# Performance work log

Measured on AMD Instinct MI355X. Metric: run time of the kernel, lower is better.

## Reference

```python
import jax, jax.numpy as jnp
import numpy as np

# ---- static config (from xib add_argument defaults / chosen production sizes) ----
B, L = 16, 50            # batch, text length
LU, KU, DIM = 60, 100, 60
V, MAXVL = 2000, 10      # vocab size, max vocab word length (J)
MIN_WL, MAX_WL = 4, 10   # min/max extracted word length
NE = MAX_WL - MIN_WL + 1 # number of len_e candidates
INS_DEL_COST = 3.5       # min_ins_del_cost
UNEXTRACTED_PROB = 0.01
CONTEXT_WEIGHT = 0.1     # weight for context (conv) log-probs
NEG = -9999.9


def setup_inputs() -> dict:
    key = jax.random.key(0)
    ks = jax.random.split(key, 8)
    unit_id_seqs = jax.random.randint(ks[0], (B, L), 0, LU)
    lengths = 10 + jax.random.randint(ks[1], (B,), 0, L - 9)  # in [10, L]
    unit_repr = jax.random.normal(ks[2], (KU, DIM), jnp.float32)
    aligner_weight = 0.1 * jax.random.normal(ks[3], (LU, KU), jnp.float32)
    conv_w = jax.random.normal(ks[4], (DIM, DIM, 3), jnp.float32) / np.sqrt(3.0 * DIM)
    conv_b = jnp.zeros((DIM,), jnp.float32)
    vocab_ids = jax.random.randint(ks[5], (V, MAXVL), 0, KU)
    vocab_lengths = MIN_WL + jax.random.randint(ks[6], (V,), 0, MAXVL - MIN_WL + 1)
    return dict(unit_id_seqs=unit_id_seqs, lengths=lengths, unit_repr=unit_repr,
                aligner_weight=aligner_weight, conv_w=conv_w, conv_b=conv_b,
                vocab_ids=vocab_ids, vocab_lengths=vocab_lengths)


def reference(unit_id_seqs, lengths, unit_repr, aligner_weight, conv_w, conv_b,
              vocab_ids, vocab_lengths):
    # ---- G2P layer: embedding-as-matmul + Conv1d over length ----
    ku_char_repr = aligner_weight @ unit_repr                 # (LU, DIM)
    emb = ku_char_repr[unit_id_seqs]                          # (B, L, DIM)
    x = jnp.swapaxes(emb, 1, 2)                               # (B, DIM, L)
    y = jax.lax.conv_general_dilated(x, conv_w, (1,), 'SAME',
                                     dimension_numbers=('NCH', 'OIH', 'NCH'))
    word_repr = jnp.swapaxes(y + conv_b[None, :, None], 1, 2)  # (B, L, DIM)
    char_log_probs = jax.nn.log_softmax(ku_char_repr @ unit_repr.T, axis=-1)  # (LU, KU)
    alignment = jnp.exp(char_log_probs)
    ctx_log_probs = jax.nn.log_softmax(word_repr @ unit_repr.T, axis=-1)      # (B, L, KU)
    # per-position substitution log prob against each known unit
    pos_lp = char_log_probs[unit_id_seqs] + CONTEXT_WEIGHT * ctx_log_probs    # (B, L, KU)
    sub = pos_lp[:, :, vocab_ids]                                             # (B, L, V, J)
    sub = jnp.pad(sub, ((0, 0), (0, MAX_WL), (0, 0), (0, 0)), constant_values=NEG)
    J = MAXVL
    # ---- edit-distance style DP over (span char i, vocab char j), vectorized
    # over (batch, start position, vocab). prev[b,s,j,v] = f[i-1][j].
    j_ar = jnp.arange(J + 1, dtype=sub.dtype)
    prev = jnp.broadcast_to((-INS_DEL_COST * j_ar)[None, None, :, None], (B, L, J + 1, V))
    vl_idx = jnp.broadcast_to(vocab_lengths[None, None, None, :].astype(jnp.int32), (B, L, 1, V))
    lls = []
    for i in range(1, MAX_WL + 1):          # fixed small loop (<=10)
        sub_i = sub[:, i - 1:i - 1 + L]     # (B, L, V, J): char at position s+i-1
        row = [jnp.full((B, L, V), -INS_DEL_COST * i, dtype=sub.dtype)]
        for j in range(1, J + 1):           # fixed small loop (<=10)
            diag = prev[:, :, j - 1, :] + sub_i[:, :, :, j - 1]
            up = prev[:, :, j, :] - INS_DEL_COST
            left = row[j - 1] - INS_DEL_COST
            row.append(jnp.maximum(diag, jnp.maximum(up, left)))
        prev = jnp.stack(row, axis=2)       # (B, L, J+1, V)
        if i >= MIN_WL:                     # matched ll for word length i
            lls.append(jnp.take_along_axis(prev, vl_idx, axis=2)[:, :, 0, :])
    ll = jnp.stack(lls, axis=2)             # (B, L, NE, V) = matches.ll
    # ---- viability mask + unextracted penalty, pick best candidate ----
    starts = jnp.arange(L)
    word_lens = MIN_WL + jnp.arange(NE)
    viable = (starts[None, :, None] + word_lens[None, None, :]) <= lengths[:, None, None]  # (B,L,NE)
    unextracted = (lengths[:, None, None] - word_lens[None, None, :]).astype(ll.dtype)     # (B,1,NE)
    score = (ll + jnp.where(viable, 0.0, NEG)[..., None]
             + (unextracted * np.log(UNEXTRACTED_PROB))[..., None, :, None][:, 0])
    flat = score.reshape(B, L * NE * V)
    best_idx = jnp.argmax(flat, axis=1)
    best_matched_ll = jnp.max(flat, axis=1)
    start = best_idx // (NE * V)
    e_idx = (best_idx // V) % NE
    best_matched_vocab = best_idx % V
    end = start + MIN_WL + e_idx - 1
    return start, end, best_matched_ll, best_matched_vocab, alignment
```

## Files before the change

### kernel.cpp

```cpp
#include <hip/hip_runtime.h>
#include <math.h>
#include <stdint.h>

#define B_ 16
#define L_ 50
#define LU_ 60
#define KU_ 100
#define DIM_ 60
#define V_ 2000
#define MAXVL_ 10
#define MIN_WL_ 4
#define MAX_WL_ 10
#define NE_ 7
#define IDC_ 3.5f
#define LOG_UNEXT_ (-4.6051701859880913680359829093687f)
#define CTXW_ 0.1f
#define NQ_ 13

#define WS_PLP  0
#define WS_BEST_BYTES (80000u * 4u)
#define BEST_STRIDE 8
#define WS_VPACK_BYTES (WS_BEST_BYTES + 1024u)

#define URP_ 61
#define CWP_ 61
#define SP2_ 208

__global__ __launch_bounds__(256) void ctx_kernel(
    const int* __restrict__ uid,
    const float* __restrict__ unit_repr,
    const float* __restrict__ aligner_w,
    const float* __restrict__ conv_w,
    const float* __restrict__ conv_b,
    const int* __restrict__ vocab_ids,
    const int* __restrict__ vocab_lengths,
    float* __restrict__ ws_plp,
    float* __restrict__ out_align,
    unsigned long long* __restrict__ g_best,
    int* __restrict__ vpack)
{
  int blk = blockIdx.x;
  int t = threadIdx.x;

  if (blk == B_ * NQ_) {
    __shared__ unsigned scnt[NE_];
    if (t < NE_) scnt[t] = 0u;
    __syncthreads();
    for (int v = t; v < V_; v += 256)
      atomicAdd(&scnt[vocab_lengths[v] - MIN_WL_], 1u);
    __syncthreads();
    if (t == 0) {
      unsigned s = 0;
      for (int e = 0; e < NE_; ++e) { unsigned c = scnt[e]; scnt[e] = s; s += c; }
    }
    __syncthreads();
    for (int v = t; v < V_; v += 256) {
      int vl = vocab_lengths[v];
      unsigned dst = atomicAdd(&scnt[vl - MIN_WL_], 1u);
      unsigned q0 = 0u, q1 = 0u, q2 = 0u;
#pragma unroll
      for (int j = 0; j < 4; ++j) q0 |= ((unsigned)vocab_ids[v * MAXVL_ + j]) << (j * 8);
#pragma unroll
      for (int j = 0; j < 4; ++j) q1 |= ((unsigned)vocab_ids[v * MAXVL_ + 4 + j]) << (j * 8);
#pragma unroll
      for (int j = 0; j < 2; ++j) q2 |= ((unsigned)vocab_ids[v * MAXVL_ + 8 + j]) << (j * 8);
      int4 w;
      w.x = (int)q0; w.y = (int)q1; w.z = (int)q2;
      w.w = (int)((unsigned)vl | ((unsigned)v << 8));
      ((int4*)vpack)[dst] = w;
    }
    return;
  }

  int b = blk / NQ_, q = blk % NQ_;
  int l0 = 4 * q;
  int npos = (l0 + 4 <= L_) ? 4 : (L_ - l0);
  int alr = (blk < LU_) ? blk : -1;

  __shared__ float s_ur[KU_ * URP_];
  __shared__ float s_cw[3 * DIM_ * CWP_];
  __shared__ float s_aw[7 * KU_];
  __shared__ float s_kx[7 * DIM_];
  __shared__ float swr[4 * DIM_];
  __shared__ float sclp[4 * KU_];
  __shared__ float sctx[4 * KU_];
  __shared__ float salg[KU_];
  __shared__ float sls[9];

  if (blk == 0 && t < B_) g_best[t * BEST_STRIDE] = 0ull;

  const float4* ur4 = (const float4*)unit_repr;
  for (int k = t; k < (KU_ * DIM_) / 4; k += 256) {
    float4 v = ur4[k];
    int i0 = 4 * k;
    s_ur[((i0 + 0) / DIM_) * URP_ + ((i0 + 0) % DIM_)] = v.x;
    s_ur[((i0 + 1) / DIM_) * URP_ + ((i0 + 1) % DIM_)] = v.y;
    s_ur[((i0 + 2) / DIM_) * URP_ + ((i0 + 2) % DIM_)] = v.z;
    s_ur[((i0 + 3) / DIM_) * URP_ + ((i0 + 3) % DIM_)] = v.w;
  }
  const float4* cw4 = (const float4*)conv_w;
  for (int k = t; k < (DIM_ * DIM_ * 3) / 4; k += 256) {
    float4 v = cw4[k];
    int i0 = 4 * k;
    float vv[4] = {v.x, v.y, v.z, v.w};
#pragma unroll
    for (int e = 0; e < 4; ++e) {
      int idx = i0 + e;
      int o = idx / (3 * DIM_), id = idx % (3 * DIM_);
      s_cw[id * CWP_ + o] = vv[e];
    }
  }
  for (int i = t; i < 7 * KU_; i += 256) {
    int m = i / KU_, k = i - m * KU_;
    float w = 0.f;
    if (m < 6) {
      int ld = l0 - 1 + m;
      if (ld >= 0 && ld < L_) {
        int u = uid[b * L_ + ld];
        w = aligner_w[u * KU_ + k];
      }
    } else if (alr >= 0) {
      w = aligner_w[alr * KU_ + k];
    }
    s_aw[i] = w;
  }
  __syncthreads();

  for (int idx = t; idx < 7 * DIM_; idx += 256) {
    int m = idx / DIM_, c = idx - m * DIM_;
    const float4* aw4 = (const float4*)&s_aw[m * KU_];
    float acc = 0.f;
    for (int k4 = 0; k4 < KU_ / 4; ++k4) {
      float4 a = aw4[k4];
      int k = 4 * k4;
      acc += a.x * s_ur[(k + 0) * URP_ + c];
      acc += a.y * s_ur[(k + 1) * URP_ + c];
      acc += a.z * s_ur[(k + 2) * URP_ + c];
      acc += a.w * s_ur[(k + 3) * URP_ + c];
    }
    s_kx[idx] = acc;
  }
  __syncthreads();

  for (int idx = t; idx < 240 + 4 * KU_; idx += 256) {
    if (idx < 240) {
      int p = idx / DIM_, o = idx - p * DIM_;
      const float4* x04 = (const float4*)&s_kx[(p + 0) * DIM_];
      const float4* x14 = (const float4*)&s_kx[(p + 1) * DIM_];
      const float4* x24 = (const float4*)&s_kx[(p + 2) * DIM_];
      float acc = conv_b[o];
      for (int i4 = 0; i4 < DIM_ / 4; ++i4) {
        float4 x0 = x04[i4], x1 = x14[i4], x2 = x24[i4];
        int i = 4 * i4;
        acc += x0.x * s_cw[((i + 0) * 3 + 0) * CWP_ + o];
        acc += x1.x * s_cw[((i + 0) * 3 + 1) * CWP_ + o];
        acc += x2.x * s_cw[((i + 0) * 3 + 2) * CWP_ + o];
        acc += x0.y * s_cw[((i + 1) * 3 + 0) * CWP_ + o];
        acc += x1.y * s_cw[((i + 1) * 3 + 1) * CWP_ + o];
        acc += x2.y * s_cw[((i + 1) * 3 + 2) * CWP_ + o];
        acc += x0.z * s_cw[((i + 2) * 3 + 0) * CWP_ + o];
        acc += x1.z * s_cw[((i + 2) * 3 + 1) * CWP_ + o];
        acc += x2.z * s_cw[((i + 2) * 3 + 2) * CWP_ + o];
        acc += x0.w * s_cw[((i + 3) * 3 + 0) * CWP_ + o];
        acc += x1.w * s_cw[((i + 3) * 3 + 1) * CWP_ + o];
        acc += x2.w * s_cw[((i + 3) * 3 + 2) * CWP_ + o];
      }
      swr[p * DIM_ + o] = acc;
    } else {
      int r = idx - 240;
      int p = r / KU_, j = r - p * KU_;
      const float4* kx4 = (const float4*)&s_kx[(p + 1) * DIM_];
      float acc = 0.f;
      for (int d4 = 0; d4 < DIM_ / 4; ++d4) {
        float4 x = kx4[d4];
        int d = 4 * d4;
        acc += x.x * s_ur[j * URP_ + d + 0];
        acc += x.y * s_ur[j * URP_ + d + 1];
        acc += x.z * s_ur[j * URP_ + d + 2];
        acc += x.w * s_ur[j * URP_ + d + 3];
      }
      sclp[r] = acc;
    }
  }
  __syncthreads();

  for (int idx = t; idx < 4 * KU_ + KU_; idx += 256) {
    if (idx < 4 * KU_) {
      int p = idx / KU_, j = idx - p * KU_;
      const float4* w4 = (const float4*)&swr[p * DIM_];
      float acc = 0.f;
      for (int d4 = 0; d4 < DIM_ / 4; ++d4) {
        float4 x = w4[d4];
        int d = 4 * d4;
        acc += x.x * s_ur[j * URP_ + d + 0];
        acc += x.y * s_ur[j * URP_ + d + 1];
        acc += x.z * s_ur[j * URP_ + d + 2];
        acc += x.w * s_ur[j * URP_ + d + 3];
      }
      sctx[idx] = acc;
    } else {
      int j = idx - 4 * KU_;
      const float4* kx4 = (const float4*)&s_kx[6 * DIM_];
      float acc = 0.f;
      for (int d4 = 0; d4 < DIM_ / 4; ++d4) {
        float4 x = kx4[d4];
        int d = 4 * d4;
        acc += x.x * s_ur[j * URP_ + d + 0];
        acc += x.y * s_ur[j * URP_ + d + 1];
        acc += x.z * s_ur[j * URP_ + d + 2];
        acc += x.w * s_ur[j * URP_ + d + 3];
      }
      salg[j] = acc;
    }
  }
  __syncthreads();

  {
    int g = t >> 5, lane = t & 31;
#pragma unroll
    for (int round = 0; round < 2; ++round) {
      int r = round * 8 + g;
      if (r < 9) {
        const float* arr = (r == 8) ? salg
                          : ((r & 1) ? &sctx[(r >> 1) * KU_] : &sclp[(r >> 1) * KU_]);
        float v1 = arr[lane];
        float v2 = arr[32 + lane];
        float v3 = arr[64 + lane];
        float v4 = (lane < KU_ - 96) ? arr[96 + lane] : -1e30f;
        float mx = fmaxf(fmaxf(v1, v2), fmaxf(v3, v4));
#pragma unroll
        for (int off = 16; off > 0; off >>= 1)
          mx = fmaxf(mx, __shfl_xor(mx, off));
        float s = expf(v1 - mx) + expf(v2 - mx) + expf(v3 - mx) +
                  ((lane < KU_ - 96) ? expf(v4 - mx) : 0.f);
#pragma unroll
        for (int off = 16; off > 0; off >>= 1)
          s += __shfl_xor(s, off);
        if (lane == 0) sls[r] = mx + logf(s);
      }
    }
  }
  __syncthreads();

  for (int idx = t; idx < 4 * KU_; idx += 256) {
    int p = idx / KU_, j = idx - p * KU_;
    if (p < npos) {
      float pos = (sclp[idx] - sls[2 * p]) + CTXW_ * (sctx[idx] - sls[2 * p + 1]);
      ws_plp[(b * L_ + l0 + p) * KU_ + j] = pos + 2.0f * IDC_;
    }
  }
  if (alr >= 0 && t < KU_)
    out_align[alr * KU_ + t] = expf(salg[t] - sls[8]);
}

template<int VL>
__device__ __forceinline__ unsigned long long dp_one(
    const float* __restrict__ spair, const int* koff8,
    int imax, int len_b, int l, int v)
{
  float D[VL + 1];
#pragma unroll
  for (int j = 0; j <= VL; ++j) D[j] = 0.f;
  float bestSc = -1e30f;
  int bestI = 0;
  const char* sb = (const char*)spair;

#pragma unroll
  for (int r2 = 0; r2 < 5; ++r2) {
    const int i1 = 2 * r2 + 1, i2 = 2 * r2 + 2;
    if (i1 <= imax) {
      float2 pv[VL];
#pragma unroll
      for (int j = 0; j < VL; ++j)
        pv[j] = *(const float2*)(sb + r2 * (SP2_ * 4) + koff8[j]);
      float left = 0.f;
#pragma unroll
      for (int j = 1; j <= VL; ++j) {
        float nv = fmaxf(D[j - 1] + pv[j - 1].x, fmaxf(D[j], left));
        D[j - 1] = left;
        left = nv;
      }
      D[VL] = left;
      if (i1 >= MIN_WL_) {
        float sc = left + ((float)(len_b - i1) * LOG_UNEXT_ - IDC_ * (float)(i1 + VL));
        if (sc > bestSc) { bestSc = sc; bestI = i1; }
      }
      if (i2 <= imax) {
        left = 0.f;
#pragma unroll
        for (int j = 1; j <= VL; ++j) {
          float nv = fmaxf(D[j - 1] + pv[j - 1].y, fmaxf(D[j], left));
          D[j - 1] = left;
          left = nv;
        }
        D[VL] = left;
        if (i2 >= MIN_WL_) {
          float sc = left + ((float)(len_b - i2) * LOG_UNEXT_ - IDC_ * (float)(i2 + VL));
          if (sc > bestSc) { bestSc = sc; bestI = i2; }
        }
      }
    }
  }
  if (bestI == 0) return 0ull;
  unsigned idx = (unsigned)(l * (NE_ * V_) + (bestI - MIN_WL_) * V_ + v);
  unsigned u = __float_as_uint(bestSc);
  u = (u & 0x80000000u) ? ~u : (u | 0x80000000u);
  return ((unsigned long long)u << 32) | (unsigned long long)(~idx);
}

__global__ __launch_bounds__(256) void dp_kernel(
    const int* __restrict__ lengths,
    const float* __restrict__ ws_plp,
    const int* __restrict__ vpack,
    unsigned long long* __restrict__ g_best)
{
  int bl = blockIdx.x;
  int b = bl / L_, l = bl % L_;
  int len_b = lengths[b];
  int imax = len_b - l;
  if (imax > MAX_WL_) imax = MAX_WL_;
  if (imax < MIN_WL_) return;

  __shared__ float spair[5 * SP2_];
  __shared__ unsigned long long swave[4];
  int t = threadIdx.x;
  if (t < 250) {
    const float4* src = (const float4*)(ws_plp + (size_t)bl * KU_);
    int r = t / 25, m = t - r * 25;
    float4 v = src[r * 25 + m];
    int r2 = r >> 1, h = r & 1;
    float* dst = &spair[r2 * SP2_ + 8 * m + h];
    dst[0] = v.x; dst[2] = v.y; dst[4] = v.z; dst[6] = v.w;
  }
  __syncthreads();

  int p = blockIdx.y * 256 + t;
  const int4* vp4 = (const int4*)vpack;
  int4 w0 = (p < V_) ? vp4[p] : make_int4(0, 0, 0, 0);
  int vlen = (int)((unsigned)w0.w & 0xFFu);
  int v0 = (int)(((unsigned)w0.w) >> 8);

  int koff8[MAXVL_];
  {
    unsigned q[3] = {(unsigned)w0.x, (unsigned)w0.y, (unsigned)w0.z};
#pragma unroll
    for (int j = 0; j < MAXVL_; ++j)
      koff8[j] = (int)((q[j >> 2] >> ((j & 3) * 8)) & 0xFFu) * 8;
  }

  unsigned long long bestKey = 0ull;
  if (vlen == 4)       bestKey = dp_one<4>(spair, koff8, imax, len_b, l, v0);
  else if (vlen == 5)  bestKey = dp_one<5>(spair, koff8, imax, len_b, l, v0);
  else if (vlen == 6)  bestKey = dp_one<6>(spair, koff8, imax, len_b, l, v0);
  else if (vlen == 7)  bestKey = dp_one<7>(spair, koff8, imax, len_b, l, v0);
  else if (vlen == 8)  bestKey = dp_one<8>(spair, koff8, imax, len_b, l, v0);
  else if (vlen == 9)  bestKey = dp_one<9>(spair, koff8, imax, len_b, l, v0);
  else if (vlen == 10) bestKey = dp_one<10>(spair, koff8, imax, len_b, l, v0);

#pragma unroll
  for (int off = 32; off > 0; off >>= 1) {
    unsigned long long o = __shfl_down(bestKey, off);
    if (o > bestKey) bestKey = o;
  }
  int wid = t >> 6;
  if ((t & 63) == 0) swave[wid] = bestKey;
  __syncthreads();
  if (t == 0) {
    unsigned long long k0 = swave[0];
    for (int w = 1; w < 4; ++w)
      if (swave[w] > k0) k0 = swave[w];
    atomicMax(g_best + (size_t)b * BEST_STRIDE, k0);
  }
}

__global__ void decode_kernel(const unsigned long long* __restrict__ g_best,
                              float* __restrict__ out)
{
  int t = threadIdx.x;
  if (t < B_) {
    unsigned long long key = g_best[t * BEST_STRIDE];
    unsigned int u = (unsigned int)(key >> 32);
    unsigned int idx = ~((unsigned int)(key & 0xFFFFFFFFull));
    unsigned int bits = (u & 0x80000000u) ? (u & 0x7FFFFFFFu) : ~u;
    float val = __uint_as_float(bits);
    int start = (int)(idx / (NE_ * V_));
    int rem = (int)(idx % (NE_ * V_));
    int e = rem / V_;
    int vv = rem % V_;
    out[t] = (float)start;
    out[B_ + t] = (float)(start + MIN_WL_ + e - 1);
    out[2 * B_ + t] = val;
    out[3 * B_ + t] = (float)vv;
  }
}

extern "C" void kernel_launch(void* const* d_in, const int* in_sizes, int n_in,
                              void* d_out, int out_size, void* d_ws, size_t ws_size,
                              hipStream_t stream)
{
  const int* uid            = (const int*)d_in[0];
  const int* lengths        = (const int*)d_in[1];
  const float* unit_repr    = (const float*)d_in[2];
  const float* aligner_w    = (const float*)d_in[3];
  const float* conv_w       = (const float*)d_in[4];
  const float* conv_b       = (const float*)d_in[5];
  const int* vocab_ids      = (const int*)d_in[6];
  const int* vocab_lengths  = (const int*)d_in[7];
  float* out = (float*)d_out;
  float* ws_f = (float*)d_ws;
  unsigned long long* g_best =
      (unsigned long long*)((char*)d_ws + WS_BEST_BYTES);
  int* vpack = (int*)((char*)d_ws + WS_VPACK_BYTES);

  ctx_kernel<<<B_ * NQ_ + 1, 256, 0, stream>>>(uid, unit_repr, aligner_w,
                                               conv_w, conv_b, vocab_ids,
                                               vocab_lengths, ws_f + WS_PLP,
                                               out + 4 * B_, g_best, vpack);
  dim3 g3(B_ * L_, 8);
  dp_kernel<<<g3, 256, 0, stream>>>(lengths, ws_f + WS_PLP, vpack, g_best);
  decode_kernel<<<1, 64, 0, stream>>>(g_best, out);
}
```

Measured before the change: 102.0 us.

## Remap DP so lanes cover start positions and waves iterate vocab words

The DP kernel now launches one block per batch row and vocab chunk. Each of the 64 lanes handles one start position, and each wave loops over ten vocab words that are uniform across the wave (loaded via readfirstlane). This removes the divergence from per-thread vocab lengths, so the length-sorting prepass is dropped and vpack is written in original order. The DP is transposed to iterate over vocab characters against all 10 text positions, and a precomputed per-lane score vector handles length viability and the unextracted penalty. In exchange each block stages 54 rows of position log-probs into shared memory, DP work runs past each row's valid length, and 14 of the 64 lanes are idle.

```diff
diff --git a/kernel.cpp b/kernel.cpp
--- a/kernel.cpp
+++ b/kernel.cpp
@@ -24,7 +24,9 @@
 
 #define URP_ 61
 #define CWP_ 61
-#define SP2_ 208
+
+#define S2_ 202
+#define NKEY_ 54
 
 __global__ __launch_bounds__(256) void ctx_kernel(
     const int* __restrict__ uid,
@@ -43,20 +45,8 @@
   int t = threadIdx.x;
 
   if (blk == B_ * NQ_) {
-    __shared__ unsigned scnt[NE_];
-    if (t < NE_) scnt[t] = 0u;
-    __syncthreads();
-    for (int v = t; v < V_; v += 256)
-      atomicAdd(&scnt[vocab_lengths[v] - MIN_WL_], 1u);
-    __syncthreads();
-    if (t == 0) {
-      unsigned s = 0;
-      for (int e = 0; e < NE_; ++e) { unsigned c = scnt[e]; scnt[e] = s; s += c; }
-    }
-    __syncthreads();
     for (int v = t; v < V_; v += 256) {
       int vl = vocab_lengths[v];
-      unsigned dst = atomicAdd(&scnt[vl - MIN_WL_], 1u);
       unsigned q0 = 0u, q1 = 0u, q2 = 0u;
 #pragma unroll
       for (int j = 0; j < 4; ++j) q0 |= ((unsigned)vocab_ids[v * MAXVL_ + j]) << (j * 8);
@@ -67,7 +57,7 @@
       int4 w;
       w.x = (int)q0; w.y = (int)q1; w.z = (int)q2;
       w.w = (int)((unsigned)vl | ((unsigned)v << 8));
-      ((int4*)vpack)[dst] = w;
+      ((int4*)vpack)[v] = w;
     }
     return;
   }
@@ -255,57 +245,49 @@
 
 template<int VL>
 __device__ __forceinline__ unsigned long long dp_one(
-    const float* __restrict__ spair, const int* koff8,
-    int imax, int len_b, int l, int v)
+    const float* __restrict__ fb,
+    unsigned q0, unsigned q1, unsigned q2,
+    const float* cvec, int lbase, int vid)
 {
-  float D[VL + 1];
-#pragma unroll
-  for (int j = 0; j <= VL; ++j) D[j] = 0.f;
+  float D[MAXVL_ + 1];
+#pragma unroll
+  for (int i = 0; i <= MAXVL_; ++i) D[i] = 0.f;
+
+#pragma unroll
+  for (int j = 0; j < VL; ++j) {
+    unsigned qq = (j < 4) ? q0 : ((j < 8) ? q1 : q2);
+    int k2 = (int)((qq >> ((j & 3) * 8)) & 0xFFu) * 2;
+    float2 p0 = *(const float2*)(fb + k2);
+    float2 p1 = *(const float2*)(fb + k2 + S2_);
+    float2 p2 = *(const float2*)(fb + k2 + 2 * S2_);
+    float2 p3 = *(const float2*)(fb + k2 + 3 * S2_);
+    float2 p4 = *(const float2*)(fb + k2 + 4 * S2_);
+    float s[MAXVL_] = {p0.x, p1.x, p2.x, p3.x, p4.x,
+                       p0.y, p1.y, p2.y, p3.y, p4.y};
+    float left = 0.f;
+#pragma unroll
+    for (int i = 1; i <= MAXVL_; ++i) {
+      float nv = fmaxf(D[i - 1] + s[i - 1], fmaxf(D[i], left));
+      D[i - 1] = left;
+      left = nv;
+    }
+    D[MAXVL_] = left;
+  }
+
   float bestSc = -1e30f;
-  int bestI = 0;
-  const char* sb = (const char*)spair;
-
-#pragma unroll
-  for (int r2 = 0; r2 < 5; ++r2) {
-    const int i1 = 2 * r2 + 1, i2 = 2 * r2 + 2;
-    if (i1 <= imax) {
-      float2 pv[VL];
-#pragma unroll
-      for (int j = 0; j < VL; ++j)
-        pv[j] = *(const float2*)(sb + r2 * (SP2_ * 4) + koff8[j]);
-      float left = 0.f;
-#pragma unroll
-      for (int j = 1; j <= VL; ++j) {
-        float nv = fmaxf(D[j - 1] + pv[j - 1].x, fmaxf(D[j], left));
-        D[j - 1] = left;
-        left = nv;
-      }
-      D[VL] = left;
-      if (i1 >= MIN_WL_) {
-        float sc = left + ((float)(len_b - i1) * LOG_UNEXT_ - IDC_ * (float)(i1 + VL));
-        if (sc > bestSc) { bestSc = sc; bestI = i1; }
-      }
-      if (i2 <= imax) {
-        left = 0.f;
-#pragma unroll
-        for (int j = 1; j <= VL; ++j) {
-          float nv = fmaxf(D[j - 1] + pv[j - 1].y, fmaxf(D[j], left));
-          D[j - 1] = left;
-          left = nv;
-        }
-        D[VL] = left;
-        if (i2 >= MIN_WL_) {
-          float sc = left + ((float)(len_b - i2) * LOG_UNEXT_ - IDC_ * (float)(i2 + VL));
-          if (sc > bestSc) { bestSc = sc; bestI = i2; }
-        }
-      }
-    }
-  }
-  if (bestI == 0) return 0ull;
-  unsigned idx = (unsigned)(l * (NE_ * V_) + (bestI - MIN_WL_) * V_ + v);
+  int bestEV = 0;
+#pragma unroll
+  for (int e = 0; e < NE_; ++e) {
+    float sc = D[MIN_WL_ + e] + cvec[e];
+    if (sc > bestSc) { bestSc = sc; bestEV = e * V_; }
+  }
+  bestSc -= IDC_ * (float)VL;
+  unsigned idx = (unsigned)(lbase + bestEV + vid);
   unsigned u = __float_as_uint(bestSc);
   u = (u & 0x80000000u) ? ~u : (u | 0x80000000u);
-  return ((unsigned long long)u << 32) | (unsigned long long)(~idx);
+  unsigned long long key =
+      ((unsigned long long)u << 32) | (unsigned long long)(~idx);
+  return (bestSc > -1e29f) ? key : 0ull;
 }
 
 __global__ __launch_bounds__(256) void dp_kernel(
@@ -314,61 +296,77 @@
     const int* __restrict__ vpack,
     unsigned long long* __restrict__ g_best)
 {
-  int bl = blockIdx.x;
-  int b = bl / L_, l = bl % L_;
+  __shared__ float sp[NKEY_ * S2_];
+  __shared__ unsigned long long swave[4];
+  int b = blockIdx.x;
+  int chunk = blockIdx.y;
+  int t = threadIdx.x;
   int len_b = lengths[b];
-  int imax = len_b - l;
-  if (imax > MAX_WL_) imax = MAX_WL_;
-  if (imax < MIN_WL_) return;
-
-  __shared__ float spair[5 * SP2_];
-  __shared__ unsigned long long swave[4];
-  int t = threadIdx.x;
-  if (t < 250) {
-    const float4* src = (const float4*)(ws_plp + (size_t)bl * KU_);
-    int r = t / 25, m = t - r * 25;
-    float4 v = src[r * 25 + m];
-    int r2 = r >> 1, h = r & 1;
-    float* dst = &spair[r2 * SP2_ + 8 * m + h];
-    dst[0] = v.x; dst[2] = v.y; dst[4] = v.z; dst[6] = v.w;
-  }
-  __syncthreads();
-
-  int p = blockIdx.y * 256 + t;
+
+  const float4* src4 = (const float4*)ws_plp;
+  for (int idx = t; idx < NKEY_ * 25; idx += 256) {
+    int key = idx / 25, m = idx - key * 25;
+    int ra = b * L_ + key;     if (ra > B_ * L_ - 1) ra = B_ * L_ - 1;
+    int rb = b * L_ + key + 5; if (rb > B_ * L_ - 1) rb = B_ * L_ - 1;
+    float4 qa = src4[ra * 25 + m];
+    float4 qb = src4[rb * 25 + m];
+    float2* dst = (float2*)&sp[key * S2_ + 8 * m];
+    dst[0] = make_float2(qa.x, qb.x);
+    dst[1] = make_float2(qa.y, qb.y);
+    dst[2] = make_float2(qa.z, qb.z);
+    dst[3] = make_float2(qa.w, qb.w);
+  }
+
+  int lane = t & 63, w = t >> 6;
+  float cvec[NE_];
+#pragma unroll
+  for (int e = 0; e < NE_; ++e) {
+    int i = MIN_WL_ + e;
+    bool ok = (lane < L_) && (i <= len_b - lane);
+    cvec[e] = ok ? ((float)(len_b - i) * LOG_UNEXT_ - IDC_ * (float)i) : -1e30f;
+  }
+  int lbase = lane * (NE_ * V_);
+  int lcl = (lane < L_) ? lane : (L_ - 1);
+  const float* fb = sp + lcl * S2_;
+  __syncthreads();
+
+  unsigned long long bestKey = 0ull;
   const int4* vp4 = (const int4*)vpack;
-  int4 w0 = (p < V_) ? vp4[p] : make_int4(0, 0, 0, 0);
-  int vlen = (int)((unsigned)w0.w & 0xFFu);
-  int v0 = (int)(((unsigned)w0.w) >> 8);
-
-  int koff8[MAXVL_];
-  {
-    unsigned q[3] = {(unsigned)w0.x, (unsigned)w0.y, (unsigned)w0.z};
-#pragma unroll
-    for (int j = 0; j < MAXVL_; ++j)
-      koff8[j] = (int)((q[j >> 2] >> ((j & 3) * 8)) & 0xFFu) * 8;
-  }
-
-  unsigned long long bestKey = 0ull;
-  if (vlen == 4)       bestKey = dp_one<4>(spair, koff8, imax, len_b, l, v0);
-  else if (vlen == 5)  bestKey = dp_one<5>(spair, koff8, imax, len_b, l, v0);
-  else if (vlen == 6)  bestKey = dp_one<6>(spair, koff8, imax, len_b, l, v0);
-  else if (vlen == 7)  bestKey = dp_one<7>(spair, koff8, imax, len_b, l, v0);
-  else if (vlen == 8)  bestKey = dp_one<8>(spair, koff8, imax, len_b, l, v0);
-  else if (vlen == 9)  bestKey = dp_one<9>(spair, koff8, imax, len_b, l, v0);
-  else if (vlen == 10) bestKey = dp_one<10>(spair, koff8, imax, len_b, l, v0);
+#pragma unroll 1
+  for (int n = 0; n < 10; ++n) {
+    int v = chunk * 40 + w * 10 + n;
+    int4 wq = vp4[v];
+    unsigned q0 = (unsigned)__builtin_amdgcn_readfirstlane(wq.x);
+    unsigned q1 = (unsigned)__builtin_amdgcn_readfirstlane(wq.y);
+    unsigned q2 = (unsigned)__builtin_amdgcn_readfirstlane(wq.z);
+    unsigned q3 = (unsigned)__builtin_amdgcn_readfirstlane(wq.w);
+    int vlen = (int)(q3 & 0xFFu);
+    int vid = (int)(q3 >> 8);
+    unsigned long long kk = 0ull;
+    switch (vlen) {
+      case 4:  kk = dp_one<4>(fb, q0, q1, q2, cvec, lbase, vid); break;
+      case 5:  kk = dp_one<5>(fb, q0, q1, q2, cvec, lbase, vid); break;
+      case 6:  kk = dp_one<6>(fb, q0, q1, q2, cvec, lbase, vid); break;
+      case 7:  kk = dp_one<7>(fb, q0, q1, q2, cvec, lbase, vid); break;
+      case 8:  kk = dp_one<8>(fb, q0, q1, q2, cvec, lbase, vid); break;
+      case 9:  kk = dp_one<9>(fb, q0, q1, q2, cvec, lbase, vid); break;
+      case 10: kk = dp_one<10>(fb, q0, q1, q2, cvec, lbase, vid); break;
+      default: break;
+    }
+    if (kk > bestKey) bestKey = kk;
+  }
 
 #pragma unroll
   for (int off = 32; off > 0; off >>= 1) {
     unsigned long long o = __shfl_down(bestKey, off);
     if (o > bestKey) bestKey = o;
   }
-  int wid = t >> 6;
-  if ((t & 63) == 0) swave[wid] = bestKey;
+  if ((t & 63) == 0) swave[w] = bestKey;
   __syncthreads();
   if (t == 0) {
     unsigned long long k0 = swave[0];
-    for (int w = 1; w < 4; ++w)
-      if (swave[w] > k0) k0 = swave[w];
+    for (int x = 1; x < 4; ++x)
+      if (swave[x] > k0) k0 = swave[x];
     atomicMax(g_best + (size_t)b * BEST_STRIDE, k0);
   }
 }
@@ -416,7 +414,7 @@
                                                conv_w, conv_b, vocab_ids,
                                                vocab_lengths, ws_f + WS_PLP,
                                                out + 4 * B_, g_best, vpack);
-  dim3 g3(B_ * L_, 8);
+  dim3 g3(B_, 50);
   dp_kernel<<<g3, 256, 0, stream>>>(lengths, ws_f + WS_PLP, vpack, g_best);
   decode_kernel<<<1, 64, 0, stream>>>(g_best, out);
 }
```

After: 106.4 us. 4.4% more time.

## Process four start positions per thread with transposed DP over vocab chars

Applied to the files above, without the earlier changes.

Restructures the edit-distance DP so each thread handles one vocab word against four consecutive start positions at once, iterating over vocab characters in the outer loop and reusing each shared-memory pair load across four DP chains. Blocks now cover a (batch, 4-start) tile with 512 threads, each looping over four vocab words with a prefetch of the next word's packed ids. This cuts the grid from 6400 blocks to 208 and amortises the log-prob loads and the vocab metadata reads. In exchange, register pressure rises because four DP arrays are live, and the fixed MAXVL-length chains do extra work for short words. Occupancy is also lower with so few blocks.

```diff
diff --git a/kernel.cpp b/kernel.cpp
--- a/kernel.cpp
+++ b/kernel.cpp
@@ -24,7 +24,9 @@
 
 #define URP_ 61
 #define CWP_ 61
-#define SP2_ 208
+
+#define S2P_ 208
+#define NROW_ 14
 
 __global__ __launch_bounds__(256) void ctx_kernel(
     const int* __restrict__ uid,
@@ -253,109 +255,126 @@
     out_align[alr * KU_ + t] = expf(salg[t] - sls[8]);
 }
 
+#define CHAIN_(Dm, MOFF)                                                 \
+  {                                                                      \
+    float left = 0.f;                                                    \
+    _Pragma("unroll")                                                    \
+    for (int i = 1; i <= MAXVL_; ++i) {                                  \
+      float nv = fmaxf(Dm[i - 1] + s[(i - 1) + (MOFF)],                  \
+                       fmaxf(Dm[i], left));                              \
+      Dm[i - 1] = left;                                                  \
+      left = nv;                                                         \
+    }                                                                    \
+    Dm[MAXVL_] = left;                                                   \
+  }
+
 template<int VL>
-__device__ __forceinline__ unsigned long long dp_one(
-    const float* __restrict__ spair, const int* koff8,
-    int imax, int len_b, int l, int v)
+__device__ __forceinline__ unsigned long long dp4_one(
+    const float* __restrict__ sp,
+    unsigned q0, unsigned q1, unsigned q2,
+    int imax0,
+    float lenLU,
+    int lbase0, int vid)
 {
-  float D[VL + 1];
-#pragma unroll
-  for (int j = 0; j <= VL; ++j) D[j] = 0.f;
-  float bestSc = -1e30f;
-  int bestI = 0;
-  const char* sb = (const char*)spair;
-
-#pragma unroll
-  for (int r2 = 0; r2 < 5; ++r2) {
-    const int i1 = 2 * r2 + 1, i2 = 2 * r2 + 2;
-    if (i1 <= imax) {
-      float2 pv[VL];
-#pragma unroll
-      for (int j = 0; j < VL; ++j)
-        pv[j] = *(const float2*)(sb + r2 * (SP2_ * 4) + koff8[j]);
-      float left = 0.f;
-#pragma unroll
-      for (int j = 1; j <= VL; ++j) {
-        float nv = fmaxf(D[j - 1] + pv[j - 1].x, fmaxf(D[j], left));
-        D[j - 1] = left;
-        left = nv;
-      }
-      D[VL] = left;
-      if (i1 >= MIN_WL_) {
-        float sc = left + ((float)(len_b - i1) * LOG_UNEXT_ - IDC_ * (float)(i1 + VL));
-        if (sc > bestSc) { bestSc = sc; bestI = i1; }
-      }
-      if (i2 <= imax) {
-        left = 0.f;
-#pragma unroll
-        for (int j = 1; j <= VL; ++j) {
-          float nv = fmaxf(D[j - 1] + pv[j - 1].y, fmaxf(D[j], left));
-          D[j - 1] = left;
-          left = nv;
-        }
-        D[VL] = left;
-        if (i2 >= MIN_WL_) {
-          float sc = left + ((float)(len_b - i2) * LOG_UNEXT_ - IDC_ * (float)(i2 + VL));
-          if (sc > bestSc) { bestSc = sc; bestI = i2; }
-        }
-      }
-    }
-  }
-  if (bestI == 0) return 0ull;
-  unsigned idx = (unsigned)(l * (NE_ * V_) + (bestI - MIN_WL_) * V_ + v);
-  unsigned u = __float_as_uint(bestSc);
-  u = (u & 0x80000000u) ? ~u : (u | 0x80000000u);
-  return ((unsigned long long)u << 32) | (unsigned long long)(~idx);
+  float D0[MAXVL_ + 1], D1[MAXVL_ + 1], D2[MAXVL_ + 1], D3[MAXVL_ + 1];
+#pragma unroll
+  for (int i = 0; i <= MAXVL_; ++i) { D0[i] = 0.f; D1[i] = 0.f; D2[i] = 0.f; D3[i] = 0.f; }
+
+#pragma unroll
+  for (int j = 0; j < VL; ++j) {
+    unsigned qq = (j < 4) ? q0 : ((j < 8) ? q1 : q2);
+    int k2 = (int)((qq >> ((j & 3) * 8)) & 0xFFu) * 2;
+    const float* fb = sp + k2;
+    float2 P0 = *(const float2*)(fb);
+    float2 P1 = *(const float2*)(fb + S2P_);
+    float2 P2 = *(const float2*)(fb + 2 * S2P_);
+    float2 P3 = *(const float2*)(fb + 3 * S2P_);
+    float2 P4 = *(const float2*)(fb + 4 * S2P_);
+    float2 P5 = *(const float2*)(fb + 5 * S2P_);
+    float2 P6 = *(const float2*)(fb + 6 * S2P_);
+    float s[NROW_] = {P0.x, P0.y, P1.x, P1.y, P2.x, P2.y, P3.x, P3.y,
+                      P4.x, P4.y, P5.x, P5.y, P6.x, P6.y};
+    CHAIN_(D0, 0)
+    CHAIN_(D1, 1)
+    CHAIN_(D2, 2)
+    CHAIN_(D3, 3)
+  }
+
+  unsigned long long bestKey = 0ull;
+#pragma unroll
+  for (int m = 0; m < 4; ++m) {
+    const float* Dm = (m == 0) ? D0 : (m == 1) ? D1 : (m == 2) ? D2 : D3;
+    int imax = imax0 - m;
+#pragma unroll
+    for (int e = 0; e < NE_; ++e) {
+      const int i = MIN_WL_ + e;
+      if (i <= imax) {
+        float cc = lenLU + (float)i * (-LOG_UNEXT_ - IDC_) - IDC_ * (float)VL;
+        float sc = Dm[i] + cc;
+        unsigned idx = (unsigned)(lbase0 + m * (NE_ * V_) + e * V_ + vid);
+        unsigned u = __float_as_uint(sc);
+        u = (u & 0x80000000u) ? ~u : (u | 0x80000000u);
+        unsigned long long key =
+            ((unsigned long long)u << 32) | (unsigned long long)(~idx);
+        if (key > bestKey) bestKey = key;
+      }
+    }
+  }
+  return bestKey;
 }
 
-__global__ __launch_bounds__(256) void dp_kernel(
+__global__ __launch_bounds__(512) void dp_kernel(
     const int* __restrict__ lengths,
     const float* __restrict__ ws_plp,
     const int* __restrict__ vpack,
     unsigned long long* __restrict__ g_best)
 {
-  int bl = blockIdx.x;
-  int b = bl / L_, l = bl % L_;
+  int blk = blockIdx.x;
+  int b = blk / NQ_, q = blk % NQ_;
+  int l0 = 4 * q;
   int len_b = lengths[b];
-  int imax = len_b - l;
-  if (imax > MAX_WL_) imax = MAX_WL_;
-  if (imax < MIN_WL_) return;
-
-  __shared__ float spair[5 * SP2_];
-  __shared__ unsigned long long swave[4];
+  int imax0 = len_b - l0;
+  if (imax0 < MIN_WL_) return;
+
+  __shared__ float sp[7 * S2P_];
+  __shared__ unsigned long long swave[8];
   int t = threadIdx.x;
-  if (t < 250) {
-    const float4* src = (const float4*)(ws_plp + (size_t)bl * KU_);
-    int r = t / 25, m = t - r * 25;
-    float4 v = src[r * 25 + m];
-    int r2 = r >> 1, h = r & 1;
-    float* dst = &spair[r2 * SP2_ + 8 * m + h];
+
+  if (t < NROW_ * 25) {
+    const float4* src4 = (const float4*)ws_plp;
+    int r = t / 25, m4 = t - r * 25;
+    int g = b * L_ + l0 + r;
+    if (g > B_ * L_ - 1) g = B_ * L_ - 1;
+    float4 v = src4[g * 25 + m4];
+    float* dst = &sp[(r >> 1) * S2P_ + 8 * m4 + (r & 1)];
     dst[0] = v.x; dst[2] = v.y; dst[4] = v.z; dst[6] = v.w;
   }
   __syncthreads();
 
-  int p = blockIdx.y * 256 + t;
+  float lenLU = (float)len_b * LOG_UNEXT_;
+  int lbase0 = l0 * (NE_ * V_);
   const int4* vp4 = (const int4*)vpack;
-  int4 w0 = (p < V_) ? vp4[p] : make_int4(0, 0, 0, 0);
-  int vlen = (int)((unsigned)w0.w & 0xFFu);
-  int v0 = (int)(((unsigned)w0.w) >> 8);
-
-  int koff8[MAXVL_];
-  {
-    unsigned q[3] = {(unsigned)w0.x, (unsigned)w0.y, (unsigned)w0.z};
-#pragma unroll
-    for (int j = 0; j < MAXVL_; ++j)
-      koff8[j] = (int)((q[j >> 2] >> ((j & 3) * 8)) & 0xFFu) * 8;
-  }
 
   unsigned long long bestKey = 0ull;
-  if (vlen == 4)       bestKey = dp_one<4>(spair, koff8, imax, len_b, l, v0);
-  else if (vlen == 5)  bestKey = dp_one<5>(spair, koff8, imax, len_b, l, v0);
-  else if (vlen == 6)  bestKey = dp_one<6>(spair, koff8, imax, len_b, l, v0);
-  else if (vlen == 7)  bestKey = dp_one<7>(spair, koff8, imax, len_b, l, v0);
-  else if (vlen == 8)  bestKey = dp_one<8>(spair, koff8, imax, len_b, l, v0);
-  else if (vlen == 9)  bestKey = dp_one<9>(spair, koff8, imax, len_b, l, v0);
-  else if (vlen == 10) bestKey = dp_one<10>(spair, koff8, imax, len_b, l, v0);
+  int4 wq = (t < V_) ? vp4[t] : make_int4(0, 0, 0, 0);
+#pragma unroll 1
+  for (int s4 = 0; s4 < 4; ++s4) {
+    int vn = t + (s4 + 1) * 512;
+    int4 wqn = (s4 < 3 && vn < V_) ? vp4[vn] : make_int4(0, 0, 0, 0);
+    unsigned q0 = (unsigned)wq.x, q1 = (unsigned)wq.y, q2 = (unsigned)wq.z;
+    int vlen = (int)((unsigned)wq.w & 0xFFu);
+    int vid = (int)(((unsigned)wq.w) >> 8);
+    unsigned long long kk = 0ull;
+    if (vlen == 4)       kk = dp4_one<4>(sp, q0, q1, q2, imax0, lenLU, lbase0, vid);
+    else if (vlen == 5)  kk = dp4_one<5>(sp, q0, q1, q2, imax0, lenLU, lbase0, vid);
+    else if (vlen == 6)  kk = dp4_one<6>(sp, q0, q1, q2, imax0, lenLU, lbase0, vid);
+    else if (vlen == 7)  kk = dp4_one<7>(sp, q0, q1, q2, imax0, lenLU, lbase0, vid);
+    else if (vlen == 8)  kk = dp4_one<8>(sp, q0, q1, q2, imax0, lenLU, lbase0, vid);
+    else if (vlen == 9)  kk = dp4_one<9>(sp, q0, q1, q2, imax0, lenLU, lbase0, vid);
+    else if (vlen == 10) kk = dp4_one<10>(sp, q0, q1, q2, imax0, lenLU, lbase0, vid);
+    if (kk > bestKey) bestKey = kk;
+    wq = wqn;
+  }
 
 #pragma unroll
   for (int off = 32; off > 0; off >>= 1) {
@@ -367,7 +386,7 @@
   __syncthreads();
   if (t == 0) {
     unsigned long long k0 = swave[0];
-    for (int w = 1; w < 4; ++w)
+    for (int w = 1; w < 8; ++w)
       if (swave[w] > k0) k0 = swave[w];
     atomicMax(g_best + (size_t)b * BEST_STRIDE, k0);
   }
@@ -416,7 +435,7 @@
                                                conv_w, conv_b, vocab_ids,
                                                vocab_lengths, ws_f + WS_PLP,
                                                out + 4 * B_, g_best, vpack);
-  dim3 g3(B_ * L_, 8);
-  dp_kernel<<<g3, 256, 0, stream>>>(lengths, ws_f + WS_PLP, vpack, g_best);
+  dp_kernel<<<B_ * NQ_, 512, 0, stream>>>(lengths, ws_f + WS_PLP, vpack,
+                                          g_best);
   decode_kernel<<<1, 64, 0, stream>>>(g_best, out);
 }
```

Result: no change. 100.0 us (-1.9%).
